# Kernel optimization log

Measured on AMD Instinct MI355X. Metric: run time of the kernel, lower is better.

Reference implementation:

```python
import jax, jax.numpy as jnp
import numpy as np

N_SEQ, L, DH, DX, M, G, N_TOK, N_MEM, N_TYP = 1024, 64, 256, 128, 8192, 4096, 10000, 262144, 64

def setup_inputs() -> dict:
    key = jax.random.key(0)
    ks = jax.random.split(key, 16)
    s_q = 1.0 / np.sqrt(2 * DH)
    s_k = 1.0 / np.sqrt(DH)
    s_r = 1.0 / np.sqrt(2 * DH + DX)
    msk = jax.random.randint(ks[4], (N_SEQ, L), 0, 2).astype(jnp.int32)
    msk = msk.at[:, 0].set(1)  # guarantee >=1 valid position per sequence
    return {
        "mem": jax.random.randint(ks[0], (N_MEM,), 0, N_TOK),
        "grp": jax.random.randint(ks[1], (N_MEM,), 0, G),
        "pos2grp": jax.random.randint(ks[2], (N_SEQ, L), 0, G),
        "h_grp": jax.random.normal(ks[3], (N_SEQ, L, DH), jnp.float32),
        "msk": msk,
        "idx": jnp.sort(jax.random.randint(ks[5], (M,), 0, N_SEQ)),
        "src": jax.random.randint(ks[6], (M,), 0, L),
        "dst": jax.random.randint(ks[7], (M,), 0, L),
        "typ": jax.random.randint(ks[8], (M, N_TYP), 0, 2).astype(jnp.int32),
        "tok_emb": jax.random.normal(ks[9], (N_TOK, DX), jnp.float32),
        "Wq": jax.random.normal(ks[10], (2 * DH, DH), jnp.float32) * s_q,
        "bq": jnp.zeros((DH,), jnp.float32),
        "Wk": jax.random.normal(ks[11], (DH, DH), jnp.float32) * s_k,
        "bk": jnp.zeros((DH,), jnp.float32),
        "Wrel": jax.random.normal(ks[12], (2 * DH + DX, N_TYP), jnp.float32) * s_r,
        "brel": jnp.zeros((N_TYP,), jnp.float32),
    }

def reference(mem, grp, pos2grp, h_grp, msk, idx, src, dst, typ,
              tok_emb, Wq, bq, Wk, bk, Wrel, brel):
    # z_grp = scatter_sum(tok_encoder(mem), grp, 0)[pos2grp]  -> (n, l, dx)
    z = jax.ops.segment_sum(tok_emb[mem], grp, num_segments=G)
    z_grp = z[pos2grp]
    # q = cat(h_grp[idx, src], h_grp[idx, dst])  -> (M, 2*dh)
    q = jnp.concatenate([h_grp[idx, src], h_grp[idx, dst]], axis=-1)
    qp = q @ Wq + bq                                    # (M, dh)
    kp = jnp.einsum('nld,de->nle', h_grp, Wk) + bk      # (n, l, dh)
    # repeat_interleave(nq) over sorted-by-group queries == gather by idx
    scores = jnp.einsum('mld,md->ml', kp[idx], qp) / jnp.sqrt(jnp.float32(DH))
    scores = jnp.where(msk[idx].astype(bool), scores, -jnp.inf)
    attn = jax.nn.softmax(scores, axis=1)               # (M, l)
    ctx = jnp.einsum('ml,mlv->mv', attn, z_grp[idx])    # (M, dx)
    logit = jnp.concatenate([q, ctx], axis=-1) @ Wrel + brel  # (M, n_typ)
    return logit
```

## Files before the change

kernel.cpp:

```cpp
#include <hip/hip_runtime.h>
#include <math.h>

#define N_SEQ 1024
#define LL 64
#define DH 256
#define DX 128
#define MQ 8192
#define GG 4096
#define NTYP 64
#define NMEM 262144

typedef __attribute__((ext_vector_type(8))) short short8v;
typedef __attribute__((ext_vector_type(4))) float float4v;

__device__ __forceinline__ unsigned short f2bf(float x) {
    unsigned int u = __float_as_uint(x);
    u += 0x7FFFu + ((u >> 16) & 1u);
    return (unsigned short)(u >> 16);
}

__global__ __launch_bounds__(256) void k_prep(const float* __restrict__ Wq,
                                              unsigned short* __restrict__ WqB,
                                              int4* __restrict__ cnt4,
                                              const int* __restrict__ idx,
                                              int* __restrict__ ofs_n) {
    int b = blockIdx.x, tid = threadIdx.x;
    if (b < 128) {
        int i = (b * 256 + tid) * 4;
        float4 v = *(const float4*)(Wq + i);
        ushort4 o;
        o.x = f2bf(v.x); o.y = f2bf(v.y); o.z = f2bf(v.z); o.w = f2bf(v.w);
        *(ushort4*)(WqB + i) = o;
    } else if (b < 132) {
        cnt4[(b - 128) * 256 + tid] = (int4){0, 0, 0, 0};
    } else {
        int n = (b - 132) * 256 + tid;
        int lo = 0, hi = MQ;
        while (lo < hi) {
            int mid = (lo + hi) >> 1;
            if (idx[mid] < n) lo = mid + 1; else hi = mid;
        }
        ofs_n[n] = lo;
        if (n == 0) ofs_n[N_SEQ] = MQ;
    }
}

__global__ __launch_bounds__(256) void k_hist(const int* __restrict__ grp,
                                              int* __restrict__ cnt,
                                              int* __restrict__ rank) {
    int i = blockIdx.x * 256 + threadIdx.x;
    if (i < NMEM) rank[i] = atomicAdd(&cnt[grp[i]], 1);
}

__global__ __launch_bounds__(1024) void k_scan(const int* __restrict__ cnt,
                                               int* __restrict__ ofs) {
    __shared__ int wsum[16];
    int tid = threadIdx.x;
    int4 c = ((const int4*)cnt)[tid];
    int local = c.x + c.y + c.z + c.w;
    int lane = tid & 63, w = tid >> 6;
    int v = local;
    for (int off = 1; off < 64; off <<= 1) {
        int t = __shfl_up(v, off);
        if (lane >= off) v += t;
    }
    if (lane == 63) wsum[w] = v;
    __syncthreads();
    if (tid < 16) {
        int s = wsum[tid];
        for (int off = 1; off < 16; off <<= 1) {
            int t = __shfl_up(s, off);
            if (tid >= off) s += t;
        }
        wsum[tid] = s;
    }
    __syncthreads();
    int base = (w > 0 ? wsum[w - 1] : 0) + (v - local);
    int4 o;
    o.x = base;
    o.y = base + c.x;
    o.z = o.y + c.y;
    o.w = o.z + c.z;
    ((int4*)ofs)[tid] = o;
}

__global__ __launch_bounds__(256) void k_permute(const int* __restrict__ grp,
                                                 const int* __restrict__ mem,
                                                 const int* __restrict__ ofs,
                                                 const int* __restrict__ rank,
                                                 int* __restrict__ tok_sorted) {
    int i = blockIdx.x * 256 + threadIdx.x;
    if (i < NMEM) tok_sorted[ofs[grp[i]] + rank[i]] = mem[i];
}

__global__ __launch_bounds__(128) void k_zsum(const int* __restrict__ ofs,
                                              const int* __restrict__ cnt,
                                              const int* __restrict__ tok_sorted,
                                              const float* __restrict__ tok_emb,
                                              const float* __restrict__ Wrel,
                                              float* __restrict__ zw) {
    __shared__ int idxs[128];
    __shared__ float red[4][128];
    __shared__ float zs[128];
    int g = blockIdx.x;
    int tid = threadIdx.x;
    int gq = tid >> 5;
    int s = tid & 31;
    int start = ofs[g], n = cnt[g];
    float4 a0 = {0.f, 0.f, 0.f, 0.f}, a1 = {0.f, 0.f, 0.f, 0.f};
    for (int j0 = 0; j0 < n; j0 += 128) {
        __syncthreads();
        int rem = n - j0;
        if (tid < rem) idxs[tid] = tok_sorted[start + j0 + tid];
        __syncthreads();
        int kmax = rem < 128 ? rem : 128;
        int k = gq;
        for (; k + 4 < kmax; k += 8) {
            const float4* r0 = (const float4*)(tok_emb + (size_t)idxs[k] * DX);
            const float4* r1 = (const float4*)(tok_emb + (size_t)idxs[k + 4] * DX);
            float4 v0 = r0[s], v1 = r1[s];
            a0.x += v0.x; a0.y += v0.y; a0.z += v0.z; a0.w += v0.w;
            a1.x += v1.x; a1.y += v1.y; a1.z += v1.z; a1.w += v1.w;
        }
        if (k < kmax) {
            const float4* r0 = (const float4*)(tok_emb + (size_t)idxs[k] * DX);
            float4 v0 = r0[s];
            a0.x += v0.x; a0.y += v0.y; a0.z += v0.z; a0.w += v0.w;
        }
    }
    a0.x += a1.x; a0.y += a1.y; a0.z += a1.z; a0.w += a1.w;
    ((float4*)red[gq])[s] = a0;
    __syncthreads();
    zs[tid] = red[0][tid] + red[1][tid] + red[2][tid] + red[3][tid];
    __syncthreads();
    if (tid < NTYP) {
        float a2s = 0.f;
#pragma unroll 8
        for (int v = 0; v < DX; ++v)
            a2s += zs[v] * Wrel[(size_t)(512 + v) * NTYP + tid];
        zw[(size_t)g * NTYP + tid] = a2s;
    }
}

__global__ __launch_bounds__(256) void k_wqkb2(const float* __restrict__ Wk,
                                               const float* __restrict__ bq,
                                               const unsigned short* __restrict__ WqB,
                                               const float* __restrict__ Wrel,
                                               const float* __restrict__ brel,
                                               unsigned short* __restrict__ BT,
                                               float* __restrict__ bias) {
    __shared__ __align__(16) unsigned short A[16 * 256];
    __shared__ float bred[16][17];
    int b = blockIdx.x;
    int tid = threadIdx.x;
    if (b < 16) {
        int n0 = b * 16;
        {
            int r = tid >> 4;
            int kc = (tid & 15) * 16;
            const float4* s4 = (const float4*)(Wk + (size_t)(n0 + r) * 256 + kc);
            unsigned short* Arow = A + r * 256;
#pragma unroll
            for (int j = 0; j < 2; ++j) {
                float4 lo = s4[j * 2], hi = s4[j * 2 + 1];
                unsigned short tmp[8];
                tmp[0] = f2bf(lo.x); tmp[1] = f2bf(lo.y);
                tmp[2] = f2bf(lo.z); tmp[3] = f2bf(lo.w);
                tmp[4] = f2bf(hi.x); tmp[5] = f2bf(hi.y);
                tmp[6] = f2bf(hi.z); tmp[7] = f2bf(hi.w);
                int c = (kc >> 3) + j;
                int cs = (c & ~7) | ((c & 7) ^ (r & 7));
                *(int4*)(Arow + cs * 8) = *(int4*)tmp;
            }
        }
        __syncthreads();
        int w = tid >> 6, lane = tid & 63;
        int r = lane & 15, kq = lane >> 4;
        float4v acc[8];
#pragma unroll
        for (int t = 0; t < 8; ++t) acc[t] = (float4v){0.f, 0.f, 0.f, 0.f};
        const unsigned short* Arow = A + r * 256;
#pragma unroll
        for (int ks = 0; ks < 8; ++ks) {
            int c = ks * 4 + kq;
            int cs = (c & ~7) | ((c & 7) ^ (r & 7));
            short8v a = *(const short8v*)(Arow + cs * 8);
            int kk = ks * 32 + kq * 8;
#pragma unroll
            for (int t = 0; t < 8; ++t) {
                int jcol = w * 128 + t * 16 + r;
                short8v bf = *(const short8v*)(WqB + (size_t)jcol * 256 + kk);
                acc[t] = __builtin_amdgcn_mfma_f32_16x16x32_bf16(a, bf, acc[t], 0, 0, 0);
            }
        }
#pragma unroll
        for (int t = 0; t < 8; ++t) {
            int jcol = w * 128 + t * 16 + r;
#pragma unroll
            for (int j = 0; j < 4; ++j)
                BT[(size_t)(n0 + kq * 4 + j) * 512 + jcol] = f2bf(acc[t][j]);
        }
        {
            int n16 = tid >> 4, seg = tid & 15;
            const float* wkr = Wk + (size_t)(n0 + n16) * 256 + seg * 16;
            const float* bqr = bq + seg * 16;
            float pb = 0.f;
#pragma unroll
            for (int i = 0; i < 16; ++i) pb += wkr[i] * bqr[i];
            bred[n16][seg] = pb;
        }
        __syncthreads();
        if (tid < 16) {
            float s = 0.f;
#pragma unroll
            for (int k2 = 0; k2 < 16; ++k2) s += bred[tid][k2];
            bias[n0 + tid] = s;
        }
    } else {
        int t0 = (b - 16) * 16;
#pragma unroll
        for (int jj = 0; jj < 2; ++jj) {
            int j = tid + jj * 256;
            const float* wr = Wrel + (size_t)j * NTYP + t0;
#pragma unroll
            for (int tt = 0; tt < 16; ++tt)
                BT[(size_t)(256 + t0 + tt) * 512 + j] = f2bf(wr[tt]);
        }
        if (b == 16 && tid < 64) bias[256 + tid] = brel[tid];
    }
}

__global__ __launch_bounds__(256) void k_gemm(const float* __restrict__ h_grp,
                                              const int* __restrict__ idx,
                                              const int* __restrict__ srcv,
                                              const int* __restrict__ dstv,
                                              const unsigned short* __restrict__ BT,
                                              const float* __restrict__ bias,
                                              unsigned short* __restrict__ qkb,
                                              float* __restrict__ part) {
    __shared__ __align__(16) unsigned short A[16 * 512];
    __shared__ int ns[16], ss[16], dsv[16];
    int bid = blockIdx.x;
    int swz = (bid & 7) * 64 + (bid >> 3);
    int m0 = swz * 16;
    int tid = threadIdx.x;
    if (tid < 16) {
        int m = m0 + tid;
        ns[tid] = idx[m];
        ss[tid] = srcv[m];
        dsv[tid] = dstv[m];
    }
    __syncthreads();
    {
        int r = tid >> 4;
        int kc = (tid & 15) * 32;
        const float* src = h_grp +
            ((size_t)ns[r] * LL + (kc < 256 ? ss[r] : dsv[r])) * DH + (kc & 255);
        const float4* s4 = (const float4*)src;
        float4 f[8];
#pragma unroll
        for (int j = 0; j < 8; ++j) f[j] = s4[j];
        unsigned short* Arow = A + r * 512;
#pragma unroll
        for (int j = 0; j < 4; ++j) {
            int c = (kc >> 3) + j;
            int cs = (c & ~7) | ((c & 7) ^ (r & 7));
            unsigned short tmp[8];
            float4 lo = f[j * 2], hi = f[j * 2 + 1];
            tmp[0] = f2bf(lo.x); tmp[1] = f2bf(lo.y);
            tmp[2] = f2bf(lo.z); tmp[3] = f2bf(lo.w);
            tmp[4] = f2bf(hi.x); tmp[5] = f2bf(hi.y);
            tmp[6] = f2bf(hi.z); tmp[7] = f2bf(hi.w);
            *(int4*)(Arow + cs * 8) = *(int4*)tmp;
        }
    }
    __syncthreads();

    int w = tid >> 6, lane = tid & 63;
    int r = lane & 15;
    int q = lane >> 4;
    int n0 = w * 80;
    float4v acc[5];
#pragma unroll
    for (int t = 0; t < 5; ++t) {
        float b = bias[n0 + t * 16 + r];
        acc[t] = (float4v){b, b, b, b};
    }
    const unsigned short* Arow = A + r * 512;
#pragma unroll 2
    for (int ks = 0; ks < 16; ++ks) {
        int c = ks * 4 + q;
        int cs = (c & ~7) | ((c & 7) ^ (r & 7));
        short8v a = *(const short8v*)(Arow + cs * 8);
        int kk = ks * 32 + q * 8;
#pragma unroll
        for (int t = 0; t < 5; ++t) {
            int n = n0 + t * 16 + r;
            short8v b = *(const short8v*)(BT + (size_t)n * 512 + kk);
            acc[t] = __builtin_amdgcn_mfma_f32_16x16x32_bf16(a, b, acc[t], 0, 0, 0);
        }
    }
#pragma unroll
    for (int t = 0; t < 5; ++t) {
        int n = n0 + t * 16 + r;
        if (n < 256) {
#pragma unroll
            for (int j = 0; j < 4; ++j)
                qkb[(size_t)(m0 + q * 4 + j) * 256 + n] = f2bf(acc[t][j]);
        } else {
#pragma unroll
            for (int j = 0; j < 4; ++j)
                part[(size_t)(m0 + q * 4 + j) * NTYP + (n - 256)] = acc[t][j];
        }
    }
}

__global__ __launch_bounds__(256) void k_attn9(const float* __restrict__ h_grp,
                                               const int* __restrict__ ofs_n,
                                               const int* __restrict__ pos2grp,
                                               const int* __restrict__ msk,
                                               const float* __restrict__ zw,
                                               const unsigned short* __restrict__ qkb,
                                               const float* __restrict__ part,
                                               float* __restrict__ out) {
    __shared__ __align__(16) unsigned short zwT[64][72];
    __shared__ __align__(16) unsigned short PsT[16][72];
    __shared__ float red0[4][16], red1[4][16];

    int bid = blockIdx.x;
    int n = (bid & 7) * 128 + (bid >> 3);
    int start = ofs_n[n];
    int nq = ofs_n[n + 1] - start;
    if (nq <= 0) return;

    int tid = threadIdx.x;
    int w = tid >> 6, lane = tid & 63;
    int q15 = lane & 15, kq = lane >> 4;

    int mk = msk[n * LL + lane];
    int gv = pos2grp[n * LL + lane];

    {
        int l = 16 * w + (lane >> 2);
        int cb = (lane & 3) * 16;
        int gl = __shfl(gv, l);
        const float4* zr4 = (const float4*)(zw + (size_t)gl * NTYP + cb);
#pragma unroll
        for (int i4 = 0; i4 < 4; ++i4) {
            float4 zv = zr4[i4];
            zwT[cb + i4 * 4 + 0][l] = f2bf(zv.x);
            zwT[cb + i4 * 4 + 1][l] = f2bf(zv.y);
            zwT[cb + i4 * 4 + 2][l] = f2bf(zv.z);
            zwT[cb + i4 * 4 + 3][l] = f2bf(zv.w);
        }
    }

    const float* hrow = h_grp + ((size_t)n * LL + 16 * w + q15) * DH;
    short8v afrag[8];
#pragma unroll
    for (int ks = 0; ks < 8; ++ks) {
        const float4* p = (const float4*)(hrow + ks * 32 + kq * 8);
        float4 f0 = p[0], f1 = p[1];
        unsigned short t[8];
        t[0] = f2bf(f0.x); t[1] = f2bf(f0.y);
        t[2] = f2bf(f0.z); t[3] = f2bf(f0.w);
// ... 50 lines not shown
#pragma unroll
        for (int ks = 0; ks < 2; ++ks) {
            short8v a = *(const short8v*)(&PsT[q15][ks * 32 + kq * 8]);
#pragma unroll
            for (int ct = 0; ct < 4; ++ct) {
                short8v b = *(const short8v*)(&zwT[ct * 16 + q15][ks * 32 + kq * 8]);
                cacc[ct] = __builtin_amdgcn_mfma_f32_16x16x32_bf16(a, b, cacc[ct], 0, 0, 0);
            }
        }
#pragma unroll
        for (int ct = 0; ct < 4; ++ct) {
            int col = ct * 16 + q15;
#pragma unroll
            for (int j = 0; j < 4; ++j) {
                int qrow2 = kq * 4 + j;
                if (qrow2 < nqt) {
                    size_t m = (size_t)(start + t0 + qrow2);
                    out[m * NTYP + col] = part[m * NTYP + col] + cacc[ct][j];
                }
            }
        }
    }
}

extern "C" void kernel_launch(void* const* d_in, const int* in_sizes, int n_in,
                              void* d_out, int out_size, void* d_ws, size_t ws_size,
                              hipStream_t stream) {
    const int*   mem     = (const int*)d_in[0];
    const int*   grp     = (const int*)d_in[1];
    const int*   pos2grp = (const int*)d_in[2];
    const float* h_grp   = (const float*)d_in[3];
    const int*   msk     = (const int*)d_in[4];
    const int*   idx     = (const int*)d_in[5];
    const int*   srcv    = (const int*)d_in[6];
    const int*   dstv    = (const int*)d_in[7];
    const float* tok_emb = (const float*)d_in[9];
    const float* Wq      = (const float*)d_in[10];
    const float* bq      = (const float*)d_in[11];
    const float* Wk      = (const float*)d_in[12];
    const float* bk      = (const float*)d_in[13];
    const float* Wrel    = (const float*)d_in[14];
    const float* brel    = (const float*)d_in[15];
    float* out = (float*)d_out;
    (void)bk;

    float* ws = (float*)d_ws;
    size_t off = 0;
    float* zw   = ws + off; off += (size_t)GG * NTYP;
    unsigned short* qkb = (unsigned short*)(ws + off); off += (size_t)MQ * 256 / 2;
    float* part = ws + off; off += (size_t)MQ * NTYP;
    float* bias = ws + off; off += 320;
    unsigned short* BT  = (unsigned short*)(ws + off); off += (320 * 512) / 2;
    unsigned short* WqB = (unsigned short*)(ws + off); off += (512 * 256) / 2;
    int* cnt        = (int*)(ws + off); off += GG;
    int* ofs        = (int*)(ws + off); off += GG;
    int* rank       = (int*)(ws + off); off += NMEM;
    int* tok_sorted = (int*)(ws + off); off += NMEM;
    int* ofs_n      = (int*)(ws + off); off += N_SEQ + 1;

    k_prep<<<136, 256, 0, stream>>>(Wq, WqB, (int4*)cnt, idx, ofs_n);

    k_hist<<<NMEM / 256, 256, 0, stream>>>(grp, cnt, rank);
    k_scan<<<1, 1024, 0, stream>>>(cnt, ofs);
    k_permute<<<NMEM / 256, 256, 0, stream>>>(grp, mem, ofs, rank, tok_sorted);
    k_zsum<<<GG, 128, 0, stream>>>(ofs, cnt, tok_sorted, tok_emb, Wrel, zw);

    k_wqkb2<<<20, 256, 0, stream>>>(Wk, bq, WqB, Wrel, brel, BT, bias);

    k_gemm<<<MQ / 16, 256, 0, stream>>>(h_grp, idx, srcv, dstv, BT, bias, qkb, part);

    k_attn9<<<N_SEQ, 256, 0, stream>>>(h_grp, ofs_n, pos2grp, msk, zw, qkb, part, out);
}
```

Measured before the change: 111.0 us.

## Precompute token-by-Wrel projections, move Wrel packing to prep, widen gemm tiles

Reorders the segment sum and the projection: every token embedding is first multiplied by the ctx slice of Wrel, giving a 10000x64 table, and k_zsum then sums these 64-wide rows per group instead of 128-wide embeddings. This halves the gathered bytes per memory entry and drops the per-group 128x64 matvec, at the cost of an extra kernel that projects all tokens. The Wrel/brel packing moves from k_wqkb2 into k_prep. k_gemm now processes 32 rows per 512-thread block so each B load is reused across two row halves.

```diff
diff --git a/kernel.cpp b/kernel.cpp
--- a/kernel.cpp
+++ b/kernel.cpp
@@ -9,6 +9,7 @@
 #define GG 4096
 #define NTYP 64
 #define NMEM 262144
+#define N_TOK 10000
 
 typedef __attribute__((ext_vector_type(8))) short short8v;
 typedef __attribute__((ext_vector_type(4))) float float4v;
@@ -23,7 +24,11 @@
                                               unsigned short* __restrict__ WqB,
                                               int4* __restrict__ cnt4,
                                               const int* __restrict__ idx,
-                                              int* __restrict__ ofs_n) {
+                                              int* __restrict__ ofs_n,
+                                              const float* __restrict__ Wrel,
+                                              const float* __restrict__ brel,
+                                              unsigned short* __restrict__ BT,
+                                              float* __restrict__ bias) {
     int b = blockIdx.x, tid = threadIdx.x;
     if (b < 128) {
         int i = (b * 256 + tid) * 4;
@@ -33,7 +38,7 @@
         *(ushort4*)(WqB + i) = o;
     } else if (b < 132) {
         cnt4[(b - 128) * 256 + tid] = (int4){0, 0, 0, 0};
-    } else {
+    } else if (b < 136) {
         int n = (b - 132) * 256 + tid;
         int lo = 0, hi = MQ;
         while (lo < hi) {
@@ -42,6 +47,17 @@
         }
         ofs_n[n] = lo;
         if (n == 0) ofs_n[N_SEQ] = MQ;
+    } else {
+        int t0 = (b - 136) * 16;
+#pragma unroll
+        for (int jj = 0; jj < 2; ++jj) {
+            int j = tid + jj * 256;
+            const float* wr = Wrel + (size_t)j * NTYP + t0;
+#pragma unroll
+            for (int tt = 0; tt < 16; ++tt)
+                BT[(size_t)(256 + t0 + tt) * 512 + j] = f2bf(wr[tt]);
+        }
+        if (b == 136 && tid < 64) bias[256 + tid] = brel[tid];
     }
 }
 
@@ -93,19 +109,30 @@
     if (i < NMEM) tok_sorted[ofs[grp[i]] + rank[i]] = mem[i];
 }
 
+__global__ __launch_bounds__(256) void k_tokw(const float* __restrict__ tok_emb,
+                                              const float* __restrict__ Wrel,
+                                              float* __restrict__ tokw) {
+    int tt = blockIdx.x * 4 + (threadIdx.x >> 6);
+    int t = threadIdx.x & 63;
+    const float* row = tok_emb + (size_t)tt * DX;
+    float acc = 0.f;
+#pragma unroll 8
+    for (int v = 0; v < DX; ++v)
+        acc += row[v] * Wrel[(size_t)(512 + v) * NTYP + t];
+    tokw[(size_t)tt * NTYP + t] = acc;
+}
+
 __global__ __launch_bounds__(128) void k_zsum(const int* __restrict__ ofs,
                                               const int* __restrict__ cnt,
                                               const int* __restrict__ tok_sorted,
-                                              const float* __restrict__ tok_emb,
-                                              const float* __restrict__ Wrel,
+                                              const float* __restrict__ tokw,
                                               float* __restrict__ zw) {
     __shared__ int idxs[128];
-    __shared__ float red[4][128];
-    __shared__ float zs[128];
+    __shared__ float red[8][64];
     int g = blockIdx.x;
     int tid = threadIdx.x;
-    int gq = tid >> 5;
-    int s = tid & 31;
+    int gq = tid >> 4;
+    int s = tid & 15;
     int start = ofs[g], n = cnt[g];
     float4 a0 = {0.f, 0.f, 0.f, 0.f}, a1 = {0.f, 0.f, 0.f, 0.f};
     for (int j0 = 0; j0 < n; j0 += 128) {
@@ -115,15 +142,15 @@
         __syncthreads();
         int kmax = rem < 128 ? rem : 128;
         int k = gq;
-        for (; k + 4 < kmax; k += 8) {
-            const float4* r0 = (const float4*)(tok_emb + (size_t)idxs[k] * DX);
-            const float4* r1 = (const float4*)(tok_emb + (size_t)idxs[k + 4] * DX);
+        for (; k + 8 < kmax; k += 16) {
+            const float4* r0 = (const float4*)(tokw + (size_t)idxs[k] * NTYP);
+            const float4* r1 = (const float4*)(tokw + (size_t)idxs[k + 8] * NTYP);
             float4 v0 = r0[s], v1 = r1[s];
             a0.x += v0.x; a0.y += v0.y; a0.z += v0.z; a0.w += v0.w;
             a1.x += v1.x; a1.y += v1.y; a1.z += v1.z; a1.w += v1.w;
         }
         if (k < kmax) {
-            const float4* r0 = (const float4*)(tok_emb + (size_t)idxs[k] * DX);
+            const float4* r0 = (const float4*)(tokw + (size_t)idxs[k] * NTYP);
             float4 v0 = r0[s];
             a0.x += v0.x; a0.y += v0.y; a0.z += v0.z; a0.w += v0.w;
         }
@@ -131,106 +158,87 @@
     a0.x += a1.x; a0.y += a1.y; a0.z += a1.z; a0.w += a1.w;
     ((float4*)red[gq])[s] = a0;
     __syncthreads();
-    zs[tid] = red[0][tid] + red[1][tid] + red[2][tid] + red[3][tid];
-    __syncthreads();
     if (tid < NTYP) {
-        float a2s = 0.f;
-#pragma unroll 8
-        for (int v = 0; v < DX; ++v)
-            a2s += zs[v] * Wrel[(size_t)(512 + v) * NTYP + tid];
-        zw[(size_t)g * NTYP + tid] = a2s;
+        float t = ((red[0][tid] + red[1][tid]) + (red[2][tid] + red[3][tid]))
+                + ((red[4][tid] + red[5][tid]) + (red[6][tid] + red[7][tid]));
+        zw[(size_t)g * NTYP + tid] = t;
     }
 }
 
 __global__ __launch_bounds__(256) void k_wqkb2(const float* __restrict__ Wk,
                                                const float* __restrict__ bq,
                                                const unsigned short* __restrict__ WqB,
-                                               const float* __restrict__ Wrel,
-                                               const float* __restrict__ brel,
                                                unsigned short* __restrict__ BT,
                                                float* __restrict__ bias) {
     __shared__ __align__(16) unsigned short A[16 * 256];
     __shared__ float bred[16][17];
     int b = blockIdx.x;
     int tid = threadIdx.x;
-    if (b < 16) {
-        int n0 = b * 16;
-        {
-            int r = tid >> 4;
-            int kc = (tid & 15) * 16;
-            const float4* s4 = (const float4*)(Wk + (size_t)(n0 + r) * 256 + kc);
-            unsigned short* Arow = A + r * 256;
-#pragma unroll
-            for (int j = 0; j < 2; ++j) {
-                float4 lo = s4[j * 2], hi = s4[j * 2 + 1];
-                unsigned short tmp[8];
-                tmp[0] = f2bf(lo.x); tmp[1] = f2bf(lo.y);
-                tmp[2] = f2bf(lo.z); tmp[3] = f2bf(lo.w);
-                tmp[4] = f2bf(hi.x); tmp[5] = f2bf(hi.y);
-                tmp[6] = f2bf(hi.z); tmp[7] = f2bf(hi.w);
-                int c = (kc >> 3) + j;
-                int cs = (c & ~7) | ((c & 7) ^ (r & 7));
-                *(int4*)(Arow + cs * 8) = *(int4*)tmp;
-            }
-        }
-        __syncthreads();
-        int w = tid >> 6, lane = tid & 63;
-        int r = lane & 15, kq = lane >> 4;
-        float4v acc[8];
-#pragma unroll
-        for (int t = 0; t < 8; ++t) acc[t] = (float4v){0.f, 0.f, 0.f, 0.f};
-        const unsigned short* Arow = A + r * 256;
-#pragma unroll
-        for (int ks = 0; ks < 8; ++ks) {
-            int c = ks * 4 + kq;
+    int n0 = b * 16;
+    {
+        int r = tid >> 4;
+        int kc = (tid & 15) * 16;
+        const float4* s4 = (const float4*)(Wk + (size_t)(n0 + r) * 256 + kc);
+        unsigned short* Arow = A + r * 256;
+#pragma unroll
+        for (int j = 0; j < 2; ++j) {
+            float4 lo = s4[j * 2], hi = s4[j * 2 + 1];
+            unsigned short tmp[8];
+            tmp[0] = f2bf(lo.x); tmp[1] = f2bf(lo.y);
+            tmp[2] = f2bf(lo.z); tmp[3] = f2bf(lo.w);
+            tmp[4] = f2bf(hi.x); tmp[5] = f2bf(hi.y);
+            tmp[6] = f2bf(hi.z); tmp[7] = f2bf(hi.w);
+            int c = (kc >> 3) + j;
             int cs = (c & ~7) | ((c & 7) ^ (r & 7));
-            short8v a = *(const short8v*)(Arow + cs * 8);
-            int kk = ks * 32 + kq * 8;
-#pragma unroll
-            for (int t = 0; t < 8; ++t) {
-                int jcol = w * 128 + t * 16 + r;
-                short8v bf = *(const short8v*)(WqB + (size_t)jcol * 256 + kk);
-                acc[t] = __builtin_amdgcn_mfma_f32_16x16x32_bf16(a, bf, acc[t], 0, 0, 0);
-            }
-        }
+            *(int4*)(Arow + cs * 8) = *(int4*)tmp;
+        }
+    }
+    __syncthreads();
+    int w = tid >> 6, lane = tid & 63;
+    int r = lane & 15, kq = lane >> 4;
+    float4v acc[8];
+#pragma unroll
+    for (int t = 0; t < 8; ++t) acc[t] = (float4v){0.f, 0.f, 0.f, 0.f};
+    const unsigned short* Arow = A + r * 256;
+#pragma unroll
+    for (int ks = 0; ks < 8; ++ks) {
+        int c = ks * 4 + kq;
+        int cs = (c & ~7) | ((c & 7) ^ (r & 7));
+        short8v a = *(const short8v*)(Arow + cs * 8);
+        int kk = ks * 32 + kq * 8;
 #pragma unroll
         for (int t = 0; t < 8; ++t) {
             int jcol = w * 128 + t * 16 + r;
-#pragma unroll
-            for (int j = 0; j < 4; ++j)
-                BT[(size_t)(n0 + kq * 4 + j) * 512 + jcol] = f2bf(acc[t][j]);
-        }
-        {
-            int n16 = tid >> 4, seg = tid & 15;
-            const float* wkr = Wk + (size_t)(n0 + n16) * 256 + seg * 16;
-            const float* bqr = bq + seg * 16;
-            float pb = 0.f;
-#pragma unroll
-            for (int i = 0; i < 16; ++i) pb += wkr[i] * bqr[i];
-            bred[n16][seg] = pb;
-        }
-        __syncthreads();
-        if (tid < 16) {
-            float s = 0.f;
-#pragma unroll
-            for (int k2 = 0; k2 < 16; ++k2) s += bred[tid][k2];
-            bias[n0 + tid] = s;
-        }
-    } else {
-        int t0 = (b - 16) * 16;
-#pragma unroll
-        for (int jj = 0; jj < 2; ++jj) {
-            int j = tid + jj * 256;
-            const float* wr = Wrel + (size_t)j * NTYP + t0;
-#pragma unroll
-            for (int tt = 0; tt < 16; ++tt)
-                BT[(size_t)(256 + t0 + tt) * 512 + j] = f2bf(wr[tt]);
-        }
-        if (b == 16 && tid < 64) bias[256 + tid] = brel[tid];
-    }
-}
-
-__global__ __launch_bounds__(256) void k_gemm(const float* __restrict__ h_grp,
+            short8v bf = *(const short8v*)(WqB + (size_t)jcol * 256 + kk);
+            acc[t] = __builtin_amdgcn_mfma_f32_16x16x32_bf16(a, bf, acc[t], 0, 0, 0);
+        }
+    }
+#pragma unroll
+    for (int t = 0; t < 8; ++t) {
+        int jcol = w * 128 + t * 16 + r;
+#pragma unroll
+        for (int j = 0; j < 4; ++j)
+            BT[(size_t)(n0 + kq * 4 + j) * 512 + jcol] = f2bf(acc[t][j]);
+    }
+    {
+        int n16 = tid >> 4, seg = tid & 15;
+        const float* wkr = Wk + (size_t)(n0 + n16) * 256 + seg * 16;
+        const float* bqr = bq + seg * 16;
+        float pb = 0.f;
+#pragma unroll
+        for (int i = 0; i < 16; ++i) pb += wkr[i] * bqr[i];
+        bred[n16][seg] = pb;
+    }
+    __syncthreads();
+    if (tid < 16) {
+        float s = 0.f;
+#pragma unroll
+        for (int k2 = 0; k2 < 16; ++k2) s += bred[tid][k2];
+        bias[n0 + tid] = s;
+    }
+}
+
+__global__ __launch_bounds__(512) void k_gemm(const float* __restrict__ h_grp,
                                               const int* __restrict__ idx,
                                               const int* __restrict__ srcv,
                                               const int* __restrict__ dstv,
@@ -238,13 +246,13 @@
                                               const float* __restrict__ bias,
                                               unsigned short* __restrict__ qkb,
                                               float* __restrict__ part) {
-    __shared__ __align__(16) unsigned short A[16 * 512];
-    __shared__ int ns[16], ss[16], dsv[16];
+    __shared__ __align__(16) unsigned short A[32 * 512];
+    __shared__ int ns[32], ss[32], dsv[32];
     int bid = blockIdx.x;
-    int swz = (bid & 7) * 64 + (bid >> 3);
-    int m0 = swz * 16;
+    int swz = (bid & 7) * 32 + (bid >> 3);
+    int m0 = swz * 32;
     int tid = threadIdx.x;
-    if (tid < 16) {
+    if (tid < 32) {
         int m = m0 + tid;
         ns[tid] = idx[m];
         ss[tid] = srcv[m];
@@ -277,20 +285,23 @@
     __syncthreads();
 
     int w = tid >> 6, lane = tid & 63;
+    int nw = w & 3;
+    int mh = w >> 2;
     int r = lane & 15;
     int q = lane >> 4;
-    int n0 = w * 80;
+    int n0 = nw * 80;
     float4v acc[5];
 #pragma unroll
     for (int t = 0; t < 5; ++t) {
         float b = bias[n0 + t * 16 + r];
         acc[t] = (float4v){b, b, b, b};
     }
-    const unsigned short* Arow = A + r * 512;
+    int arow = mh * 16 + r;
+    const unsigned short* Arow = A + arow * 512;
 #pragma unroll 2
     for (int ks = 0; ks < 16; ++ks) {
         int c = ks * 4 + q;
-        int cs = (c & ~7) | ((c & 7) ^ (r & 7));
+        int cs = (c & ~7) | ((c & 7) ^ (arow & 7));
         short8v a = *(const short8v*)(Arow + cs * 8);
         int kk = ks * 32 + q * 8;
 #pragma unroll
@@ -306,11 +317,11 @@
         if (n < 256) {
 #pragma unroll
             for (int j = 0; j < 4; ++j)
-                qkb[(size_t)(m0 + q * 4 + j) * 256 + n] = f2bf(acc[t][j]);
+                qkb[(size_t)(m0 + mh * 16 + q * 4 + j) * 256 + n] = f2bf(acc[t][j]);
         } else {
 #pragma unroll
             for (int j = 0; j < 4; ++j)
-                part[(size_t)(m0 + q * 4 + j) * NTYP + (n - 256)] = acc[t][j];
+                part[(size_t)(m0 + mh * 16 + q * 4 + j) * NTYP + (n - 256)] = acc[t][j];
         }
     }
 }
@@ -467,22 +478,26 @@
     float* bias = ws + off; off += 320;
     unsigned short* BT  = (unsigned short*)(ws + off); off += (320 * 512) / 2;
     unsigned short* WqB = (unsigned short*)(ws + off); off += (512 * 256) / 2;
+    float* tokw = ws + off; off += (size_t)N_TOK * NTYP;
     int* cnt        = (int*)(ws + off); off += GG;
     int* ofs        = (int*)(ws + off); off += GG;
     int* rank       = (int*)(ws + off); off += NMEM;
     int* tok_sorted = (int*)(ws + off); off += NMEM;
     int* ofs_n      = (int*)(ws + off); off += N_SEQ + 1;
 
-    k_prep<<<136, 256, 0, stream>>>(Wq, WqB, (int4*)cnt, idx, ofs_n);
+    k_prep<<<140, 256, 0, stream>>>(Wq, WqB, (int4*)cnt, idx, ofs_n,
+                                    Wrel, brel, BT, bias);
 
     k_hist<<<NMEM / 256, 256, 0, stream>>>(grp, cnt, rank);
     k_scan<<<1, 1024, 0, stream>>>(cnt, ofs);
     k_permute<<<NMEM / 256, 256, 0, stream>>>(grp, mem, ofs, rank, tok_sorted);
-    k_zsum<<<GG, 128, 0, stream>>>(ofs, cnt, tok_sorted, tok_emb, Wrel, zw);
-
-    k_wqkb2<<<20, 256, 0, stream>>>(Wk, bq, WqB, Wrel, brel, BT, bias);
-
-    k_gemm<<<MQ / 16, 256, 0, stream>>>(h_grp, idx, srcv, dstv, BT, bias, qkb, part);
+
+    k_tokw<<<N_TOK / 4, 256, 0, stream>>>(tok_emb, Wrel, tokw);
+    k_zsum<<<GG, 128, 0, stream>>>(ofs, cnt, tok_sorted, tokw, zw);
+
+    k_wqkb2<<<16, 256, 0, stream>>>(Wk, bq, WqB, BT, bias);
+
+    k_gemm<<<MQ / 32, 512, 0, stream>>>(h_grp, idx, srcv, dstv, BT, bias, qkb, part);
 
     k_attn9<<<N_SEQ, 256, 0, stream>>>(h_grp, ofs_n, pos2grp, msk, zw, qkb, part, out);
 }
```

Result: slower. 127.4 us (+14.7%).

## Fuse histogram, scan, permute, zsum and weight prep into one persistent kernel

Applied to the files above, without the earlier changes.

Replaces the separate hist, scan, permute, zsum and weight-prep kernels with a single 512-block kernel that uses a software grid barrier (atomic counter plus generation) between phases. Each block handles 512 memory entries and 8 groups, and the scan runs as a 256-thread single-block phase. The aim is to remove several kernel launch gaps and tail effects. In exchange it relies on all 512 blocks being co-resident to avoid deadlock, and it spends spin-wait time at each barrier.

```diff
diff --git a/kernel.cpp b/kernel.cpp
--- a/kernel.cpp
+++ b/kernel.cpp
@@ -9,6 +9,7 @@
 #define GG 4096
 #define NTYP 64
 #define NMEM 262144
+#define NB_ZP 512
 
 typedef __attribute__((ext_vector_type(8))) short short8v;
 typedef __attribute__((ext_vector_type(4))) float float4v;
@@ -19,11 +20,28 @@
     return (unsigned short)(u >> 16);
 }
 
-__global__ __launch_bounds__(256) void k_prep(const float* __restrict__ Wq,
+__device__ __forceinline__ void gbar(int* bcnt, int* bgen, int gen) {
+    __syncthreads();
+    if (threadIdx.x == 0) {
+        __threadfence();
+        if (atomicAdd(bcnt, 1) == NB_ZP - 1) {
+            atomicExch(bcnt, 0);
+            __threadfence();
+            atomicAdd(bgen, 1);
+        } else {
+            while (atomicAdd(bgen, 0) < gen) __builtin_amdgcn_s_sleep(2);
+        }
+        __threadfence();
+    }
+    __syncthreads();
+}
+
+__global__ __launch_bounds__(256) void k_init(const float* __restrict__ Wq,
                                               unsigned short* __restrict__ WqB,
                                               int4* __restrict__ cnt4,
                                               const int* __restrict__ idx,
-                                              int* __restrict__ ofs_n) {
+                                              int* __restrict__ ofs_n,
+                                              int* __restrict__ bar) {
     int b = blockIdx.x, tid = threadIdx.x;
     if (b < 128) {
         int i = (b * 256 + tid) * 4;
@@ -34,6 +52,7 @@
     } else if (b < 132) {
         cnt4[(b - 128) * 256 + tid] = (int4){0, 0, 0, 0};
     } else {
+        if (b == 132 && tid < 2) bar[tid] = 0;
         int n = (b - 132) * 256 + tid;
         int lo = 0, hi = MQ;
         while (lo < hi) {
@@ -45,115 +64,28 @@
     }
 }
 
-__global__ __launch_bounds__(256) void k_hist(const int* __restrict__ grp,
-                                              int* __restrict__ cnt,
-                                              int* __restrict__ rank) {
-    int i = blockIdx.x * 256 + threadIdx.x;
-    if (i < NMEM) rank[i] = atomicAdd(&cnt[grp[i]], 1);
-}
-
-__global__ __launch_bounds__(1024) void k_scan(const int* __restrict__ cnt,
-                                               int* __restrict__ ofs) {
-    __shared__ int wsum[16];
-    int tid = threadIdx.x;
-    int4 c = ((const int4*)cnt)[tid];
-    int local = c.x + c.y + c.z + c.w;
+__global__ __launch_bounds__(256, 2) void k_zpath(
+        const int* __restrict__ grp, const int* __restrict__ mem,
+        int* __restrict__ cnt, int* __restrict__ ofs,
+        int* __restrict__ rank, int* __restrict__ tok_sorted,
+        const float* __restrict__ tok_emb, const float* __restrict__ Wrel,
+        float* __restrict__ zw,
+        const float* __restrict__ Wk, const float* __restrict__ bq,
+        const unsigned short* __restrict__ WqB, const float* __restrict__ brel,
+        unsigned short* __restrict__ BT, float* __restrict__ bias,
+        int* __restrict__ bar) {
+    __shared__ __align__(16) unsigned char smem[9344];
+    int b = blockIdx.x, tid = threadIdx.x;
     int lane = tid & 63, w = tid >> 6;
-    int v = local;
-    for (int off = 1; off < 64; off <<= 1) {
-        int t = __shfl_up(v, off);
-        if (lane >= off) v += t;
-    }
-    if (lane == 63) wsum[w] = v;
-    __syncthreads();
-    if (tid < 16) {
-        int s = wsum[tid];
-        for (int off = 1; off < 16; off <<= 1) {
-            int t = __shfl_up(s, off);
-            if (tid >= off) s += t;
-        }
-        wsum[tid] = s;
-    }
-    __syncthreads();
-    int base = (w > 0 ? wsum[w - 1] : 0) + (v - local);
-    int4 o;
-    o.x = base;
-    o.y = base + c.x;
-    o.z = o.y + c.y;
-    o.w = o.z + c.z;
-    ((int4*)ofs)[tid] = o;
-}
-
-__global__ __launch_bounds__(256) void k_permute(const int* __restrict__ grp,
-                                                 const int* __restrict__ mem,
-                                                 const int* __restrict__ ofs,
-                                                 const int* __restrict__ rank,
-                                                 int* __restrict__ tok_sorted) {
-    int i = blockIdx.x * 256 + threadIdx.x;
-    if (i < NMEM) tok_sorted[ofs[grp[i]] + rank[i]] = mem[i];
-}
-
-__global__ __launch_bounds__(128) void k_zsum(const int* __restrict__ ofs,
-                                              const int* __restrict__ cnt,
-                                              const int* __restrict__ tok_sorted,
-                                              const float* __restrict__ tok_emb,
-                                              const float* __restrict__ Wrel,
-                                              float* __restrict__ zw) {
-    __shared__ int idxs[128];
-    __shared__ float red[4][128];
-    __shared__ float zs[128];
-    int g = blockIdx.x;
-    int tid = threadIdx.x;
-    int gq = tid >> 5;
-    int s = tid & 31;
-    int start = ofs[g], n = cnt[g];
-    float4 a0 = {0.f, 0.f, 0.f, 0.f}, a1 = {0.f, 0.f, 0.f, 0.f};
-    for (int j0 = 0; j0 < n; j0 += 128) {
-        __syncthreads();
-        int rem = n - j0;
-        if (tid < rem) idxs[tid] = tok_sorted[start + j0 + tid];
-        __syncthreads();
-        int kmax = rem < 128 ? rem : 128;
-        int k = gq;
-        for (; k + 4 < kmax; k += 8) {
-            const float4* r0 = (const float4*)(tok_emb + (size_t)idxs[k] * DX);
-            const float4* r1 = (const float4*)(tok_emb + (size_t)idxs[k + 4] * DX);
-            float4 v0 = r0[s], v1 = r1[s];
-            a0.x += v0.x; a0.y += v0.y; a0.z += v0.z; a0.w += v0.w;
-            a1.x += v1.x; a1.y += v1.y; a1.z += v1.z; a1.w += v1.w;
-        }
-        if (k < kmax) {
-            const float4* r0 = (const float4*)(tok_emb + (size_t)idxs[k] * DX);
-            float4 v0 = r0[s];
-            a0.x += v0.x; a0.y += v0.y; a0.z += v0.z; a0.w += v0.w;
-        }
-    }
-    a0.x += a1.x; a0.y += a1.y; a0.z += a1.z; a0.w += a1.w;
-    ((float4*)red[gq])[s] = a0;
-    __syncthreads();
-    zs[tid] = red[0][tid] + red[1][tid] + red[2][tid] + red[3][tid];
-    __syncthreads();
-    if (tid < NTYP) {
-        float a2s = 0.f;
-#pragma unroll 8
-        for (int v = 0; v < DX; ++v)
-            a2s += zs[v] * Wrel[(size_t)(512 + v) * NTYP + tid];
-        zw[(size_t)g * NTYP + tid] = a2s;
-    }
-}
-
-__global__ __launch_bounds__(256) void k_wqkb2(const float* __restrict__ Wk,
-                                               const float* __restrict__ bq,
-                                               const unsigned short* __restrict__ WqB,
-                                               const float* __restrict__ Wrel,
-                                               const float* __restrict__ brel,
-                                               unsigned short* __restrict__ BT,
-                                               float* __restrict__ bias) {
-    __shared__ __align__(16) unsigned short A[16 * 256];
-    __shared__ float bred[16][17];
-    int b = blockIdx.x;
-    int tid = threadIdx.x;
+
+#pragma unroll
+    for (int ii = 0; ii < 2; ++ii) {
+        int i = b * 512 + ii * 256 + tid;
+        rank[i] = atomicAdd(&cnt[grp[i]], 1);
+    }
     if (b < 16) {
+        unsigned short* A = (unsigned short*)smem;
+        float (*bred)[17] = (float(*)[17])(smem + 8192);
         int n0 = b * 16;
         {
             int r = tid >> 4;
@@ -174,7 +106,6 @@
             }
         }
         __syncthreads();
-        int w = tid >> 6, lane = tid & 63;
         int r = lane & 15, kq = lane >> 4;
         float4v acc[8];
 #pragma unroll
@@ -216,7 +147,7 @@
             for (int k2 = 0; k2 < 16; ++k2) s += bred[tid][k2];
             bias[n0 + tid] = s;
         }
-    } else {
+    } else if (b < 20) {
         int t0 = (b - 16) * 16;
 #pragma unroll
         for (int jj = 0; jj < 2; ++jj) {
@@ -227,6 +158,84 @@
                 BT[(size_t)(256 + t0 + tt) * 512 + j] = f2bf(wr[tt]);
         }
         if (b == 16 && tid < 64) bias[256 + tid] = brel[tid];
+    }
+    gbar(bar, bar + 1, 1);
+
+    if (b == 0) {
+        int* wsum = (int*)smem;
+        int c[16];
+        int tsum = 0;
+        int base0 = tid * 16;
+#pragma unroll
+        for (int j = 0; j < 16; ++j) { c[j] = cnt[base0 + j]; tsum += c[j]; }
+        int v = tsum;
+        for (int o2 = 1; o2 < 64; o2 <<= 1) {
+            int t = __shfl_up(v, o2);
+            if (lane >= o2) v += t;
+        }
+        if (lane == 63) wsum[w] = v;
+        __syncthreads();
+        int wb = 0;
+#pragma unroll
+        for (int q2 = 0; q2 < 4; ++q2) if (q2 < w) wb += wsum[q2];
+        int base = wb + v - tsum;
+#pragma unroll
+        for (int j = 0; j < 16; ++j) { ofs[base0 + j] = base; base += c[j]; }
+    }
+    gbar(bar, bar + 1, 2);
+
+#pragma unroll
+    for (int ii = 0; ii < 2; ++ii) {
+        int i = b * 512 + ii * 256 + tid;
+        tok_sorted[ofs[grp[i]] + rank[i]] = mem[i];
+    }
+    gbar(bar, bar + 1, 3);
+
+    {
+        int* idxs = (int*)smem;
+        float (*red)[128] = (float(*)[128])(smem + 1024);
+        float* zs = (float*)(smem + 5120);
+        int gq = tid >> 5, s = tid & 31;
+        for (int gg = 0; gg < 8; ++gg) {
+            int g = b * 8 + gg;
+            int startg = ofs[g], n = cnt[g];
+            float4 a0 = {0.f, 0.f, 0.f, 0.f}, a1 = {0.f, 0.f, 0.f, 0.f};
+            for (int j0 = 0; j0 < n; j0 += 256) {
+                __syncthreads();
+                int rem = n - j0;
+                if (tid < rem) idxs[tid] = tok_sorted[startg + j0 + tid];
+                __syncthreads();
+                int kmax = rem < 256 ? rem : 256;
+                int k = gq;
+                for (; k + 8 < kmax; k += 16) {
+                    const float4* r0 = (const float4*)(tok_emb + (size_t)idxs[k] * DX);
+                    const float4* r1 = (const float4*)(tok_emb + (size_t)idxs[k + 8] * DX);
+                    float4 v0 = r0[s], v1 = r1[s];
+                    a0.x += v0.x; a0.y += v0.y; a0.z += v0.z; a0.w += v0.w;
+                    a1.x += v1.x; a1.y += v1.y; a1.z += v1.z; a1.w += v1.w;
+                }
+                if (k < kmax) {
+                    const float4* r0 = (const float4*)(tok_emb + (size_t)idxs[k] * DX);
+                    float4 v0 = r0[s];
+                    a0.x += v0.x; a0.y += v0.y; a0.z += v0.z; a0.w += v0.w;
+                }
+            }
+            a0.x += a1.x; a0.y += a1.y; a0.z += a1.z; a0.w += a1.w;
+            ((float4*)red[gq])[s] = a0;
+            __syncthreads();
+            if (tid < 128)
+                zs[tid] = ((red[0][tid] + red[1][tid]) + (red[2][tid] + red[3][tid]))
+                        + ((red[4][tid] + red[5][tid]) + (red[6][tid] + red[7][tid]));
+            __syncthreads();
+            if (tid < NTYP) {
+                float a2s = 0.f;
+#pragma unroll 8
+                for (int v = 0; v < DX; ++v)
+                    a2s += zs[v] * Wrel[(size_t)(512 + v) * NTYP + tid];
+                zw[(size_t)g * NTYP + tid] = a2s;
+            }
+            __syncthreads();
+        }
     }
 }
 
@@ -472,15 +481,13 @@
     int* rank       = (int*)(ws + off); off += NMEM;
     int* tok_sorted = (int*)(ws + off); off += NMEM;
     int* ofs_n      = (int*)(ws + off); off += N_SEQ + 1;
-
-    k_prep<<<136, 256, 0, stream>>>(Wq, WqB, (int4*)cnt, idx, ofs_n);
-
-    k_hist<<<NMEM / 256, 256, 0, stream>>>(grp, cnt, rank);
-    k_scan<<<1, 1024, 0, stream>>>(cnt, ofs);
-    k_permute<<<NMEM / 256, 256, 0, stream>>>(grp, mem, ofs, rank, tok_sorted);
-    k_zsum<<<GG, 128, 0, stream>>>(ofs, cnt, tok_sorted, tok_emb, Wrel, zw);
-
-    k_wqkb2<<<20, 256, 0, stream>>>(Wk, bq, WqB, Wrel, brel, BT, bias);
+    int* bar        = (int*)(ws + off); off += 4;
+
+    k_init<<<136, 256, 0, stream>>>(Wq, WqB, (int4*)cnt, idx, ofs_n, bar);
+
+    k_zpath<<<NB_ZP, 256, 0, stream>>>(grp, mem, cnt, ofs, rank, tok_sorted,
+                                       tok_emb, Wrel, zw, Wk, bq, WqB, brel,
+                                       BT, bias, bar);
 
     k_gemm<<<MQ / 16, 256, 0, stream>>>(h_grp, idx, srcv, dstv, BT, bias, qkb, part);
 
```

Result: slower. 249.2 us (+124.4%).

## Merge weight-prep into histogram kernel and zsum with query GEMM

Applied to the files above, without the earlier changes.

Folds the Wk·Wq/Wrel weight preparation blocks into the histogram launch, and merges the group-sum kernel with the query GEMM kernel as extra blocks of one grid. The zsum path now uses 256 threads with eight row-groups per block. This removes two kernel launches and lets independent work run concurrently on idle CUs, at the cost of larger shared memory per block and heterogeneous blocks sharing one launch configuration.

```diff
diff --git a/kernel.cpp b/kernel.cpp
--- a/kernel.cpp
+++ b/kernel.cpp
@@ -19,7 +19,7 @@
     return (unsigned short)(u >> 16);
 }
 
-__global__ __launch_bounds__(256) void k_prep(const float* __restrict__ Wq,
+__global__ __launch_bounds__(256) void k_init(const float* __restrict__ Wq,
                                               unsigned short* __restrict__ WqB,
                                               int4* __restrict__ cnt4,
                                               const int* __restrict__ idx,
@@ -45,11 +45,100 @@
     }
 }
 
-__global__ __launch_bounds__(256) void k_hist(const int* __restrict__ grp,
-                                              int* __restrict__ cnt,
-                                              int* __restrict__ rank) {
-    int i = blockIdx.x * 256 + threadIdx.x;
-    if (i < NMEM) rank[i] = atomicAdd(&cnt[grp[i]], 1);
+__global__ __launch_bounds__(256) void k_histw(const int* __restrict__ grp,
+                                               int* __restrict__ cnt,
+                                               int* __restrict__ rank,
+                                               const float* __restrict__ Wk,
+                                               const float* __restrict__ bq,
+                                               const unsigned short* __restrict__ WqB,
+                                               const float* __restrict__ Wrel,
+                                               const float* __restrict__ brel,
+                                               unsigned short* __restrict__ BT,
+                                               float* __restrict__ bias) {
+    __shared__ __align__(16) unsigned short A[16 * 256];
+    __shared__ float bred[16][17];
+    int b = blockIdx.x, tid = threadIdx.x;
+    if (b < 1024) {
+        int i = b * 256 + tid;
+        rank[i] = atomicAdd(&cnt[grp[i]], 1);
+        return;
+    }
+    int b2 = b - 1024;
+    if (b2 < 16) {
+        int n0 = b2 * 16;
+        {
+            int r = tid >> 4;
+            int kc = (tid & 15) * 16;
+            const float4* s4 = (const float4*)(Wk + (size_t)(n0 + r) * 256 + kc);
+            unsigned short* Arow = A + r * 256;
+#pragma unroll
+            for (int j = 0; j < 2; ++j) {
+                float4 lo = s4[j * 2], hi = s4[j * 2 + 1];
+                unsigned short tmp[8];
+                tmp[0] = f2bf(lo.x); tmp[1] = f2bf(lo.y);
+                tmp[2] = f2bf(lo.z); tmp[3] = f2bf(lo.w);
+                tmp[4] = f2bf(hi.x); tmp[5] = f2bf(hi.y);
+                tmp[6] = f2bf(hi.z); tmp[7] = f2bf(hi.w);
+                int c = (kc >> 3) + j;
+                int cs = (c & ~7) | ((c & 7) ^ (r & 7));
+                *(int4*)(Arow + cs * 8) = *(int4*)tmp;
+            }
+        }
+        __syncthreads();
+        int w = tid >> 6, lane = tid & 63;
+        int r = lane & 15, kq = lane >> 4;
+        float4v acc[8];
+#pragma unroll
+        for (int t = 0; t < 8; ++t) acc[t] = (float4v){0.f, 0.f, 0.f, 0.f};
+        const unsigned short* Arow = A + r * 256;
+#pragma unroll
+        for (int ks = 0; ks < 8; ++ks) {
+            int c = ks * 4 + kq;
+            int cs = (c & ~7) | ((c & 7) ^ (r & 7));
+            short8v a = *(const short8v*)(Arow + cs * 8);
+            int kk = ks * 32 + kq * 8;
+#pragma unroll
+            for (int t = 0; t < 8; ++t) {
+                int jcol = w * 128 + t * 16 + r;
+                short8v bf = *(const short8v*)(WqB + (size_t)jcol * 256 + kk);
+                acc[t] = __builtin_amdgcn_mfma_f32_16x16x32_bf16(a, bf, acc[t], 0, 0, 0);
+            }
+        }
+#pragma unroll
+        for (int t = 0; t < 8; ++t) {
+            int jcol = w * 128 + t * 16 + r;
+#pragma unroll
+            for (int j = 0; j < 4; ++j)
+                BT[(size_t)(n0 + kq * 4 + j) * 512 + jcol] = f2bf(acc[t][j]);
+        }
+        {
+            int n16 = tid >> 4, seg = tid & 15;
+            const float* wkr = Wk + (size_t)(n0 + n16) * 256 + seg * 16;
+            const float* bqr = bq + seg * 16;
+            float pb = 0.f;
+#pragma unroll
+            for (int i = 0; i < 16; ++i) pb += wkr[i] * bqr[i];
+            bred[n16][seg] = pb;
+        }
+        __syncthreads();
+        if (tid < 16) {
+            float s = 0.f;
+#pragma unroll
+            for (int k2 = 0; k2 < 16; ++k2) s += bred[tid][k2];
+            bias[n0 + tid] = s;
+        }
+    } else {
+        int t0 = (b2 - 16) * 16;
+#pragma unroll
+        for (int jj = 0; jj < 2; ++jj) {
+            int j = tid + jj * 256;
+            const float* wr = Wrel + (size_t)j * NTYP + t0;
+#pragma unroll
+            for (int tt = 0; tt < 16; ++tt)
+                BT[(size_t)(256 + t0 + tt) * 512 + j] = f2bf(wr[tt]);
+        }
+        if (b2 == 16 && tid < 64) bias[256 + tid] = brel[tid];
+    }
 }
 
 __global__ __launch_bounds__(1024) void k_scan(const int* __restrict__ cnt,
@@ -93,157 +182,73 @@
     if (i < NMEM) tok_sorted[ofs[grp[i]] + rank[i]] = mem[i];
 }
 
-__global__ __launch_bounds__(128) void k_zsum(const int* __restrict__ ofs,
-                                              const int* __restrict__ cnt,
-                                              const int* __restrict__ tok_sorted,
-                                              const float* __restrict__ tok_emb,
-                                              const float* __restrict__ Wrel,
-                                              float* __restrict__ zw) {
-    __shared__ int idxs[128];
-    __shared__ float red[4][128];
-    __shared__ float zs[128];
-    int g = blockIdx.x;
-    int tid = threadIdx.x;
-    int gq = tid >> 5;
-    int s = tid & 31;
-    int start = ofs[g], n = cnt[g];
-    float4 a0 = {0.f, 0.f, 0.f, 0.f}, a1 = {0.f, 0.f, 0.f, 0.f};
-    for (int j0 = 0; j0 < n; j0 += 128) {
-        __syncthreads();
-        int rem = n - j0;
-        if (tid < rem) idxs[tid] = tok_sorted[start + j0 + tid];
-        __syncthreads();
-        int kmax = rem < 128 ? rem : 128;
-        int k = gq;
-        for (; k + 4 < kmax; k += 8) {
-            const float4* r0 = (const float4*)(tok_emb + (size_t)idxs[k] * DX);
-            const float4* r1 = (const float4*)(tok_emb + (size_t)idxs[k + 4] * DX);
-            float4 v0 = r0[s], v1 = r1[s];
-            a0.x += v0.x; a0.y += v0.y; a0.z += v0.z; a0.w += v0.w;
-            a1.x += v1.x; a1.y += v1.y; a1.z += v1.z; a1.w += v1.w;
-        }
-        if (k < kmax) {
-            const float4* r0 = (const float4*)(tok_emb + (size_t)idxs[k] * DX);
-            float4 v0 = r0[s];
-            a0.x += v0.x; a0.y += v0.y; a0.z += v0.z; a0.w += v0.w;
-        }
-    }
-    a0.x += a1.x; a0.y += a1.y; a0.z += a1.z; a0.w += a1.w;
-    ((float4*)red[gq])[s] = a0;
-    __syncthreads();
-    zs[tid] = red[0][tid] + red[1][tid] + red[2][tid] + red[3][tid];
-    __syncthreads();
-    if (tid < NTYP) {
-        float a2s = 0.f;
+__global__ __launch_bounds__(256) void k_zg(const int* __restrict__ ofs,
+                                            const int* __restrict__ cnt,
+                                            const int* __restrict__ tok_sorted,
+                                            const float* __restrict__ tok_emb,
+                                            const float* __restrict__ Wrel,
+                                            float* __restrict__ zw,
+                                            const float* __restrict__ h_grp,
+                                            const int* __restrict__ idx,
+                                            const int* __restrict__ srcv,
+                                            const int* __restrict__ dstv,
+                                            const unsigned short* __restrict__ BT,
+                                            const float* __restrict__ bias,
+                                            unsigned short* __restrict__ qkb,
+                                            float* __restrict__ part) {
+    __shared__ __align__(16) unsigned char smem[16896];
+    int b = blockIdx.x, tid = threadIdx.x;
+    if (b < GG) {
+        int* idxs = (int*)smem;
+        float (*red)[128] = (float(*)[128])(smem + 1024);
+        float* zs = (float*)(smem + 5120);
+        int g = b;
+        int gq = tid >> 5, s = tid & 31;
+        int startg = ofs[g], n = cnt[g];
+        float4 a0 = {0.f, 0.f, 0.f, 0.f}, a1 = {0.f, 0.f, 0.f, 0.f};
+        for (int j0 = 0; j0 < n; j0 += 256) {
+            __syncthreads();
+            int rem = n - j0;
+            if (tid < rem) idxs[tid] = tok_sorted[startg + j0 + tid];
+            __syncthreads();
+            int kmax = rem < 256 ? rem : 256;
+            int k = gq;
+            for (; k + 8 < kmax; k += 16) {
+                const float4* r0 = (const float4*)(tok_emb + (size_t)idxs[k] * DX);
+                const float4* r1 = (const float4*)(tok_emb + (size_t)idxs[k + 8] * DX);
+                float4 v0 = r0[s], v1 = r1[s];
+                a0.x += v0.x; a0.y += v0.y; a0.z += v0.z; a0.w += v0.w;
+                a1.x += v1.x; a1.y += v1.y; a1.z += v1.z; a1.w += v1.w;
+            }
+            if (k < kmax) {
+                const float4* r0 = (const float4*)(tok_emb + (size_t)idxs[k] * DX);
+                float4 v0 = r0[s];
+                a0.x += v0.x; a0.y += v0.y; a0.z += v0.z; a0.w += v0.w;
+            }
+        }
+        a0.x += a1.x; a0.y += a1.y; a0.z += a1.z; a0.w += a1.w;
+        ((float4*)red[gq])[s] = a0;
+        __syncthreads();
+        if (tid < 128)
+            zs[tid] = ((red[0][tid] + red[1][tid]) + (red[2][tid] + red[3][tid]))
+                    + ((red[4][tid] + red[5][tid]) + (red[6][tid] + red[7][tid]));
+        __syncthreads();
+        if (tid < NTYP) {
+            float a2s = 0.f;
 #pragma unroll 8
-        for (int v = 0; v < DX; ++v)
-            a2s += zs[v] * Wrel[(size_t)(512 + v) * NTYP + tid];
-        zw[(size_t)g * NTYP + tid] = a2s;
-    }
-}
-
-__global__ __launch_bounds__(256) void k_wqkb2(const float* __restrict__ Wk,
-                                               const float* __restrict__ bq,
-                                               const unsigned short* __restrict__ WqB,
-                                               const float* __restrict__ Wrel,
-                                               const float* __restrict__ brel,
-                                               unsigned short* __restrict__ BT,
-                                               float* __restrict__ bias) {
-    __shared__ __align__(16) unsigned short A[16 * 256];
-    __shared__ float bred[16][17];
-    int b = blockIdx.x;
-    int tid = threadIdx.x;
-    if (b < 16) {
-        int n0 = b * 16;
-        {
-            int r = tid >> 4;
-            int kc = (tid & 15) * 16;
-            const float4* s4 = (const float4*)(Wk + (size_t)(n0 + r) * 256 + kc);
-            unsigned short* Arow = A + r * 256;
-#pragma unroll
-            for (int j = 0; j < 2; ++j) {
-                float4 lo = s4[j * 2], hi = s4[j * 2 + 1];
-                unsigned short tmp[8];
-                tmp[0] = f2bf(lo.x); tmp[1] = f2bf(lo.y);
-                tmp[2] = f2bf(lo.z); tmp[3] = f2bf(lo.w);
-                tmp[4] = f2bf(hi.x); tmp[5] = f2bf(hi.y);
-                tmp[6] = f2bf(hi.z); tmp[7] = f2bf(hi.w);
-                int c = (kc >> 3) + j;
-                int cs = (c & ~7) | ((c & 7) ^ (r & 7));
-                *(int4*)(Arow + cs * 8) = *(int4*)tmp;
-            }
-        }
-        __syncthreads();
-        int w = tid >> 6, lane = tid & 63;
-        int r = lane & 15, kq = lane >> 4;
-        float4v acc[8];
-#pragma unroll
-        for (int t = 0; t < 8; ++t) acc[t] = (float4v){0.f, 0.f, 0.f, 0.f};
-        const unsigned short* Arow = A + r * 256;
-#pragma unroll
-        for (int ks = 0; ks < 8; ++ks) {
-            int c = ks * 4 + kq;
-            int cs = (c & ~7) | ((c & 7) ^ (r & 7));
-            short8v a = *(const short8v*)(Arow + cs * 8);
-            int kk = ks * 32 + kq * 8;
-#pragma unroll
-            for (int t = 0; t < 8; ++t) {
-                int jcol = w * 128 + t * 16 + r;
-                short8v bf = *(const short8v*)(WqB + (size_t)jcol * 256 + kk);
-                acc[t] = __builtin_amdgcn_mfma_f32_16x16x32_bf16(a, bf, acc[t], 0, 0, 0);
-            }
-        }
-#pragma unroll
-        for (int t = 0; t < 8; ++t) {
-            int jcol = w * 128 + t * 16 + r;
-#pragma unroll
-            for (int j = 0; j < 4; ++j)
-                BT[(size_t)(n0 + kq * 4 + j) * 512 + jcol] = f2bf(acc[t][j]);
-        }
-        {
-            int n16 = tid >> 4, seg = tid & 15;
-            const float* wkr = Wk + (size_t)(n0 + n16) * 256 + seg * 16;
-            const float* bqr = bq + seg * 16;
-            float pb = 0.f;
-#pragma unroll
-            for (int i = 0; i < 16; ++i) pb += wkr[i] * bqr[i];
-            bred[n16][seg] = pb;
-        }
-        __syncthreads();
-        if (tid < 16) {
-            float s = 0.f;
-#pragma unroll
-            for (int k2 = 0; k2 < 16; ++k2) s += bred[tid][k2];
-            bias[n0 + tid] = s;
-        }
-    } else {
-        int t0 = (b - 16) * 16;
-#pragma unroll
-        for (int jj = 0; jj < 2; ++jj) {
-            int j = tid + jj * 256;
-            const float* wr = Wrel + (size_t)j * NTYP + t0;
-#pragma unroll
-            for (int tt = 0; tt < 16; ++tt)
-                BT[(size_t)(256 + t0 + tt) * 512 + j] = f2bf(wr[tt]);
-        }
-        if (b == 16 && tid < 64) bias[256 + tid] = brel[tid];
-    }
-}
-
-__global__ __launch_bounds__(256) void k_gemm(const float* __restrict__ h_grp,
-                                              const int* __restrict__ idx,
-                                              const int* __restrict__ srcv,
-                                              const int* __restrict__ dstv,
-                                              const unsigned short* __restrict__ BT,
-                                              const float* __restrict__ bias,
-                                              unsigned short* __restrict__ qkb,
-                                              float* __restrict__ part) {
-    __shared__ __align__(16) unsigned short A[16 * 512];
-    __shared__ int ns[16], ss[16], dsv[16];
-    int bid = blockIdx.x;
+            for (int v = 0; v < DX; ++v)
+                a2s += zs[v] * Wrel[(size_t)(512 + v) * NTYP + tid];
+            zw[(size_t)g * NTYP + tid] = a2s;
+        }
+        return;
+    }
+    unsigned short* A = (unsigned short*)smem;
+    int* ns  = (int*)(smem + 16384);
+    int* ss  = (int*)(smem + 16448);
+    int* dsv = (int*)(smem + 16512);
+    int bid = b - GG;
     int swz = (bid & 7) * 64 + (bid >> 3);
     int m0 = swz * 16;
-    int tid = threadIdx.x;
     if (tid < 16) {
         int m = m0 + tid;
         ns[tid] = idx[m];
@@ -283,8 +288,8 @@
     float4v acc[5];
 #pragma unroll
     for (int t = 0; t < 5; ++t) {
-        float b = bias[n0 + t * 16 + r];
-        acc[t] = (float4v){b, b, b, b};
+        float bb = bias[n0 + t * 16 + r];
+        acc[t] = (float4v){bb, bb, bb, bb};
     }
     const unsigned short* Arow = A + r * 512;
 #pragma unroll 2
@@ -296,8 +301,8 @@
 #pragma unroll
         for (int t = 0; t < 5; ++t) {
             int n = n0 + t * 16 + r;
-            short8v b = *(const short8v*)(BT + (size_t)n * 512 + kk);
-            acc[t] = __builtin_amdgcn_mfma_f32_16x16x32_bf16(a, b, acc[t], 0, 0, 0);
+            short8v bb = *(const short8v*)(BT + (size_t)n * 512 + kk);
+            acc[t] = __builtin_amdgcn_mfma_f32_16x16x32_bf16(a, bb, acc[t], 0, 0, 0);
         }
     }
 #pragma unroll
@@ -473,16 +478,16 @@
     int* tok_sorted = (int*)(ws + off); off += NMEM;
     int* ofs_n      = (int*)(ws + off); off += N_SEQ + 1;
 
-    k_prep<<<136, 256, 0, stream>>>(Wq, WqB, (int4*)cnt, idx, ofs_n);
-
-    k_hist<<<NMEM / 256, 256, 0, stream>>>(grp, cnt, rank);
+    k_init<<<136, 256, 0, stream>>>(Wq, WqB, (int4*)cnt, idx, ofs_n);
+
+    k_histw<<<1044, 256, 0, stream>>>(grp, cnt, rank, Wk, bq, WqB, Wrel, brel,
+                                      BT, bias);
+
     k_scan<<<1, 1024, 0, stream>>>(cnt, ofs);
     k_permute<<<NMEM / 256, 256, 0, stream>>>(grp, mem, ofs, rank, tok_sorted);
-    k_zsum<<<GG, 128, 0, stream>>>(ofs, cnt, tok_sorted, tok_emb, Wrel, zw);
-
-    k_wqkb2<<<20, 256, 0, stream>>>(Wk, bq, WqB, Wrel, brel, BT, bias);
-
-    k_gemm<<<MQ / 16, 256, 0, stream>>>(h_grp, idx, srcv, dstv, BT, bias, qkb, part);
+
+    k_zg<<<GG + 512, 256, 0, stream>>>(ofs, cnt, tok_sorted, tok_emb, Wrel, zw,
+                                       h_grp, idx, srcv, dstv, BT, bias, qkb, part);
 
     k_attn9<<<N_SEQ, 256, 0, stream>>>(h_grp, ofs_n, pos2grp, msk, zw, qkb, part, out);
 }
```

Measured after the change: 118.3 us. +6.6%, slower.
